# Optimization experiments

Measured on AMD Instinct MI355X. Metric: run time of the kernel, lower is better.

Reference implementation:

```python
import jax, jax.numpy as jnp
import numpy as np

N, V, I, O, G = 16, 4096, 128, 128, 16


def setup_inputs() -> dict:
    key = jax.random.key(0)
    ks = jax.random.split(key, 7)
    stdv = 1.0 / np.sqrt(O)  # reset_parameters: uniform(-stdv, stdv)
    u = lambda k, shape: jax.random.uniform(k, shape, jnp.float32, -stdv, stdv)
    return {
        "x": jax.random.normal(ks[0], (N, V, I), jnp.float32),
        "hx": jax.random.normal(ks[1], (N, V, O), jnp.float32),
        "group_index": jax.random.randint(ks[2], (V,), 0, G),
        "weight_ih": u(ks[3], (3, G, O, I)),
        "bias_ih": u(ks[4], (3, G, O)),
        "weight_hh": u(ks[5], (3, G, O, O)),
        "bias_hh": u(ks[6], (3, G, O)),
    }


def reference(x, hx, group_index, weight_ih, bias_ih, weight_hh, bias_hh):
    # gather per-node weights: [3, V, O, I] / [3, V, O]
    w_ih = weight_ih[:, group_index]
    b_ih = bias_ih[:, group_index]
    w_hh = weight_hh[:, group_index]
    b_hh = bias_hh[:, group_index]

    def lin_x(xx, w, b):  # [N,V,I] x [V,O,I] -> [N,V,O]
        return jnp.einsum("nvi,voi->nvo", xx, w) + b[None]

    def lin_h(h, w, b):  # torch einsum 'NVO,VOO->NVO' takes diagonal of w
        wd = jnp.diagonal(w, axis1=-2, axis2=-1)  # [V,O]
        return h * wd[None] + b[None]

    r = jax.nn.sigmoid(lin_x(x, w_ih[0], b_ih[0]) + lin_h(hx, w_hh[0], b_hh[0]))
    z = jax.nn.sigmoid(lin_x(x, w_ih[1], b_ih[1]) + lin_h(hx, w_hh[1], b_hh[1]))
    n = jnp.tanh(lin_x(x, w_ih[2], b_ih[2]) + r * lin_h(hx, w_hh[2], b_hh[2]))
    return (1.0 - z) * n + z * hx
```

## Files before the change

kernel.cpp:

```cpp
#include <hip/hip_runtime.h>
#include <math.h>

#define NN 16
#define VV 4096
#define II 128
#define OO 128
#define GG 16

typedef __attribute__((ext_vector_type(8))) short bf16x8;
typedef __attribute__((ext_vector_type(4))) float f32x4;

__device__ inline unsigned short f2bf(float f) {
    union { float f; unsigned u; } c; c.f = f;
    unsigned r = c.u + 0x7FFFu + ((c.u >> 16) & 1u);
    return (unsigned short)(r >> 16);
}
__device__ inline float bf2f(unsigned short h) {
    union { unsigned u; float f; } c; c.u = ((unsigned)h) << 16;
    return c.f;
}
__device__ inline void split1(float f, unsigned short& hi, unsigned short& lo) {
    hi = f2bf(f);
    lo = f2bf(f - bf2f(hi));
}
__device__ inline bf16x8 as_bf(uint4 u) {
    union { uint4 u; bf16x8 b; } c; c.u = u; return c.b;
}
__device__ inline void pack8(const float4& a, const float4& b, uint4& ph, uint4& pl) {
    unsigned short hi[8], lo[8];
    split1(a.x, hi[0], lo[0]); split1(a.y, hi[1], lo[1]);
    split1(a.z, hi[2], lo[2]); split1(a.w, hi[3], lo[3]);
    split1(b.x, hi[4], lo[4]); split1(b.y, hi[5], lo[5]);
    split1(b.z, hi[6], lo[6]); split1(b.w, hi[7], lo[7]);
    ph.x = (unsigned)hi[0] | ((unsigned)hi[1] << 16);
    ph.y = (unsigned)hi[2] | ((unsigned)hi[3] << 16);
    ph.z = (unsigned)hi[4] | ((unsigned)hi[5] << 16);
    ph.w = (unsigned)hi[6] | ((unsigned)hi[7] << 16);
    pl.x = (unsigned)lo[0] | ((unsigned)lo[1] << 16);
    pl.y = (unsigned)lo[2] | ((unsigned)lo[3] << 16);
    pl.z = (unsigned)lo[4] | ((unsigned)lo[5] << 16);
    pl.w = (unsigned)lo[6] | ((unsigned)lo[7] << 16);
}

__global__ __launch_bounds__(256) void prepack_kernel(
    const float* __restrict__ w_ih, uint4* __restrict__ wp)
{
    const int t  = blockIdx.x * 256 + threadIdx.x;
    const int i8 = t & 15;
    const int o  = (t >> 4) & 127;
    const int gg = t >> 11;

    const float* src = w_ih + ((size_t)gg * OO + o) * II + i8 * 8;
    const float4 a = *(const float4*)src;
    const float4 b = *(const float4*)(src + 4);
    uint4 ph, pl;
    pack8(a, b, ph, pl);

    const int s    = i8 >> 2;
    const int kb   = i8 & 3;
    const int lane = kb * 16 + (o & 15);
    const int ct   = o >> 4;
    const int pidx = ((gg * 8 + ct) * 4 + s) * 64 + lane;
    wp[pidx * 2]     = ph;
    wp[pidx * 2 + 1] = pl;
}

template <bool PREPACKED>
__global__ __launch_bounds__(256, 4) void ggru_mfma_kernel(
    const float* __restrict__ x,
    const float* __restrict__ hx,
    const int*   __restrict__ gidx,
    const uint4* __restrict__ wp,
    const float* __restrict__ w_ih,
    const float* __restrict__ b_ih,
    const float* __restrict__ w_hh,
    const float* __restrict__ b_hh,
    float*       __restrict__ out)
{
    const int v    = blockIdx.x;
    const int tid  = threadIdx.x;
    const int lane = tid & 63;
    const int wv   = tid >> 6;
    const int g    = gidx[v];

    __shared__ uint4 xhS[256];
    __shared__ uint4 xlS[256];

    {
        const int row = tid >> 4;
        const int sk  = tid & 15;
        const int s   = sk >> 2, kb = sk & 3;
        const float* xp = x + ((size_t)row * VV + v) * II + s * 32 + kb * 8;
        const float4 xa = *(const float4*)xp;
        const float4 xb = *(const float4*)(xp + 4);
        uint4 ph, pl;
        pack8(xa, xb, ph, pl);
        xhS[s * 64 + kb * 16 + row] = ph;
        xlS[s * 64 + kb * 16 + row] = pl;
    }
    __syncthreads();

    int tb[3][2];
    const float* wraw[3][2];
    #pragma unroll
    for (int ga = 0; ga < 3; ++ga) {
        #pragma unroll
        for (int t = 0; t < 2; ++t) {
            const int ct = wv * 2 + t;
            tb[ga][t] = ((ga * GG + g) * 8 + ct) * 4;
            wraw[ga][t] = w_ih + (((size_t)ga * GG + g) * OO + ct * 16 + (lane & 15)) * II
                          + (lane >> 4) * 8;
        }
    }

    f32x4 acc[3][2];
    #pragma unroll
    for (int ga = 0; ga < 3; ++ga)
        #pragma unroll
        for (int t = 0; t < 2; ++t)
            acc[ga][t] = (f32x4){0.f, 0.f, 0.f, 0.f};

    #pragma unroll
    for (int s = 0; s < 4; ++s) {
        const bf16x8 ah = as_bf(xhS[s * 64 + lane]);
        const bf16x8 al = as_bf(xlS[s * 64 + lane]);

        uint4 wh6[6], wl6[6];
        if (PREPACKED) {
            #pragma unroll
            for (int ga = 0; ga < 3; ++ga) {
                #pragma unroll
                for (int t = 0; t < 2; ++t) {
                    const size_t base = (size_t)(tb[ga][t] + s) * 128 + lane * 2;
                    wh6[ga * 2 + t] = wp[base];
                    wl6[ga * 2 + t] = wp[base + 1];
                }
            }
        } else {
            #pragma unroll
            for (int ga = 0; ga < 3; ++ga) {
                #pragma unroll
                for (int t = 0; t < 2; ++t) {
                    const float4 wa = *(const float4*)(wraw[ga][t] + s * 32);
                    const float4 wb = *(const float4*)(wraw[ga][t] + s * 32 + 4);
                    pack8(wa, wb, wh6[ga * 2 + t], wl6[ga * 2 + t]);
                }
            }
        }

        #pragma unroll
        for (int ga = 0; ga < 3; ++ga) {
            #pragma unroll
            for (int t = 0; t < 2; ++t) {
                const bf16x8 wh = as_bf(wh6[ga * 2 + t]);
                const bf16x8 wl = as_bf(wl6[ga * 2 + t]);
                acc[ga][t] = __builtin_amdgcn_mfma_f32_16x16x32_bf16(ah, wh, acc[ga][t], 0, 0, 0);
                acc[ga][t] = __builtin_amdgcn_mfma_f32_16x16x32_bf16(al, wh, acc[ga][t], 0, 0, 0);
                acc[ga][t] = __builtin_amdgcn_mfma_f32_16x16x32_bf16(ah, wl, acc[ga][t], 0, 0, 0);
            }
        }
    }

    const int l15 = lane & 15;
    const int rg  = lane >> 4;
    #pragma unroll
    for (int t = 0; t < 2; ++t) {
        const int o = wv * 32 + t * 16 + l15;

        const float bi0 = b_ih[(0 * GG + g) * OO + o];
        const float bi1 = b_ih[(1 * GG + g) * OO + o];
        const float bi2 = b_ih[(2 * GG + g) * OO + o];
        const float bh0 = b_hh[(0 * GG + g) * OO + o];
        const float bh1 = b_hh[(1 * GG + g) * OO + o];
        const float bh2 = b_hh[(2 * GG + g) * OO + o];
        const float wd0 = w_hh[((size_t)(0 * GG + g) * OO + o) * OO + o];
        const float wd1 = w_hh[((size_t)(1 * GG + g) * OO + o) * OO + o];
        const float wd2 = w_hh[((size_t)(2 * GG + g) * OO + o) * OO + o];

        #pragma unroll
        for (int r = 0; r < 4; ++r) {
            const int row = rg * 4 + r;
            const size_t idx = ((size_t)row * VV + v) * OO + o;
            const float h = hx[idx];

            const float gr  = acc[0][t][r] + bi0 + fmaf(h, wd0, bh0);
            const float gz  = acc[1][t][r] + bi1 + fmaf(h, wd1, bh1);
            const float ghn = fmaf(h, wd2, bh2);

            const float rr = 1.f / (1.f + __expf(-gr));
            const float zz = 1.f / (1.f + __expf(-gz));

            float tt = acc[2][t][r] + bi2 + rr * ghn;
            tt = fminf(fmaxf(tt, -15.f), 15.f);
            const float e2 = __expf(2.f * tt);
            const float th = (e2 - 1.f) / (e2 + 1.f);

            out[idx] = (1.f - zz) * th + zz * h;
        }
    }
}

extern "C" void kernel_launch(void* const* d_in, const int* in_sizes, int n_in,
                              void* d_out, int out_size, void* d_ws, size_t ws_size,
                              hipStream_t stream) {
    const float* x    = (const float*)d_in[0];
    const float* hx   = (const float*)d_in[1];
    const int*   gidx = (const int*)d_in[2];
    const float* w_ih = (const float*)d_in[3];
    const float* b_ih = (const float*)d_in[4];
    const float* w_hh = (const float*)d_in[5];
    const float* b_hh = (const float*)d_in[6];
    float* out = (float*)d_out;
    uint4* wp  = (uint4*)d_ws;

    const size_t need = 98304ull * 32ull;
    if (ws_size >= need) {
        prepack_kernel<<<384, 256, 0, stream>>>(w_ih, wp);
        ggru_mfma_kernel<true><<<VV, 256, 0, stream>>>(
            x, hx, gidx, wp, w_ih, b_ih, w_hh, b_hh, out);
    } else {
        ggru_mfma_kernel<false><<<VV, 256, 0, stream>>>(
            x, hx, gidx, (const uint4*)nullptr, w_ih, b_ih, w_hh, b_hh, out);
    }
}
```

Measured before the change: 172.7 us.

## Bucket nodes by group and share LDS-staged weights across four nodes per block

Adds a single-block bucketing kernel that sorts node indices by group into a padded list, so each 512-thread block processes four nodes from the same group. Per-group prepacked weights are staged once per k-step into LDS and reused by all four nodes, replacing per-node global weight loads and cutting weight traffic about fourfold. In exchange it adds a serial one-block bucket kernel launch, extra __syncthreads per k-step, padding blocks with idle waves, and more LDS use that may limit occupancy.

Result: faster. 162.4 us (-6.0%).

```diff
diff --git a/kernel.cpp b/kernel.cpp
--- a/kernel.cpp
+++ b/kernel.cpp
@@ -6,6 +6,10 @@
 #define II 128
 #define OO 128
 #define GG 16
+
+#define VPB   4
+#define LISTN 4144
+#define NBLK  1036
 
 typedef __attribute__((ext_vector_type(8))) short bf16x8;
 typedef __attribute__((ext_vector_type(4))) float f32x4;
@@ -42,6 +46,29 @@
     pl.w = (unsigned)lo[6] | ((unsigned)lo[7] << 16);
 }
 
+__global__ __launch_bounds__(256) void bucket_kernel(
+    const int* __restrict__ gidx, int* __restrict__ list)
+{
+    __shared__ int cnt[GG], base[GG], cur[GG];
+    const int tid = threadIdx.x;
+    if (tid < GG) cnt[tid] = 0;
+    __syncthreads();
+    for (int v = tid; v < VV; v += 256) atomicAdd(&cnt[gidx[v]], 1);
+    __syncthreads();
+    if (tid == 0) {
+        int o = 0;
+        for (int g = 0; g < GG; ++g) { base[g] = o; o += (cnt[g] + VPB - 1) & ~(VPB - 1); }
+    }
+    __syncthreads();
+    if (tid < GG) cur[tid] = base[tid];
+    for (int i = tid; i < LISTN; i += 256) list[i] = -1;
+    __syncthreads();
+    for (int v = tid; v < VV; v += 256) {
+        const int pos = atomicAdd(&cur[gidx[v]], 1);
+        list[pos] = v;
+    }
+}
+
 __global__ __launch_bounds__(256) void prepack_kernel(
     const float* __restrict__ w_ih, uint4* __restrict__ wp)
 {
@@ -65,17 +92,148 @@
     wp[pidx * 2 + 1] = pl;
 }
 
-template <bool PREPACKED>
-__global__ __launch_bounds__(256, 4) void ggru_mfma_kernel(
+__global__ __launch_bounds__(512, 4) void ggru_gemm_kernel(
     const float* __restrict__ x,
     const float* __restrict__ hx,
     const int*   __restrict__ gidx,
     const uint4* __restrict__ wp,
-    const float* __restrict__ w_ih,
+    const int*   __restrict__ list,
     const float* __restrict__ b_ih,
     const float* __restrict__ w_hh,
     const float* __restrict__ b_hh,
     float*       __restrict__ out)
+{
+    const int b    = blockIdx.x;
+    const int tid  = threadIdx.x;
+    const int lane = tid & 63;
+    const int wv   = tid >> 6;
+    const int vv   = wv >> 1;
+    const int half = wv & 1;
+
+    const int v0 = list[b * VPB];
+    if (v0 < 0) return;
+    const int g = gidx[v0];
+
+    int vl[VPB];
+    #pragma unroll
+    for (int k = 0; k < VPB; ++k) vl[k] = list[b * VPB + k];
+    const int myv = vl[vv];
+
+    __shared__ uint4 xhS[VPB][256];
+    __shared__ uint4 xlS[VPB][256];
+    __shared__ uint4 whS[1536];
+    __shared__ uint4 wlS[1536];
+
+    {
+        const int tv    = tid >> 7;
+        const int inner = tid & 127;
+        const int row   = inner >> 3;
+        const int q     = inner & 7;
+        const int s     = q >> 1;
+        const int kb0   = (q & 1) * 2;
+        const int xv    = vl[tv];
+        if (xv >= 0) {
+            const float* xp = x + ((size_t)row * VV + xv) * II + q * 16;
+            const float4 a0 = ((const float4*)xp)[0];
+            const float4 a1 = ((const float4*)xp)[1];
+            const float4 a2 = ((const float4*)xp)[2];
+            const float4 a3 = ((const float4*)xp)[3];
+            uint4 h0, l0, h1, l1;
+            pack8(a0, a1, h0, l0);
+            pack8(a2, a3, h1, l1);
+            xhS[tv][s * 64 + kb0 * 16 + row]       = h0;
+            xlS[tv][s * 64 + kb0 * 16 + row]       = l0;
+            xhS[tv][s * 64 + (kb0 + 1) * 16 + row] = h1;
+            xlS[tv][s * 64 + (kb0 + 1) * 16 + row] = l1;
+        }
+    }
+
+    f32x4 acc[3][4];
+    #pragma unroll
+    for (int ga = 0; ga < 3; ++ga)
+        #pragma unroll
+        for (int cc = 0; cc < 4; ++cc)
+            acc[ga][cc] = (f32x4){0.f, 0.f, 0.f, 0.f};
+
+    for (int s = 0; s < 4; ++s) {
+        __syncthreads();
+        #pragma unroll
+        for (int j = 0; j < 3; ++j) {
+            const int idx = j * 512 + tid;
+            const int c   = idx >> 6;
+            const int l   = idx & 63;
+            const int ga  = c >> 3;
+            const int ct  = c & 7;
+            const size_t P = ((size_t)(((ga * GG + g) * 8 + ct) * 4 + s)) * 64 + l;
+            whS[idx] = wp[2 * P];
+            wlS[idx] = wp[2 * P + 1];
+        }
+        __syncthreads();
+        if (myv >= 0) {
+            const bf16x8 ah = as_bf(xhS[vv][s * 64 + lane]);
+            const bf16x8 al = as_bf(xlS[vv][s * 64 + lane]);
+            #pragma unroll
+            for (int ga = 0; ga < 3; ++ga) {
+                #pragma unroll
+                for (int cc = 0; cc < 4; ++cc) {
+                    const int c = ga * 8 + half * 4 + cc;
+                    const bf16x8 wh = as_bf(whS[c * 64 + lane]);
+                    const bf16x8 wl = as_bf(wlS[c * 64 + lane]);
+                    acc[ga][cc] = __builtin_amdgcn_mfma_f32_16x16x32_bf16(ah, wh, acc[ga][cc], 0, 0, 0);
+                    acc[ga][cc] = __builtin_amdgcn_mfma_f32_16x16x32_bf16(al, wh, acc[ga][cc], 0, 0, 0);
+                    acc[ga][cc] = __builtin_amdgcn_mfma_f32_16x16x32_bf16(ah, wl, acc[ga][cc], 0, 0, 0);
+                }
+            }
+        }
+    }
+
+    if (myv < 0) return;
+
+    const int l15 = lane & 15;
+    const int rg  = lane >> 4;
+    #pragma unroll
+    for (int cc = 0; cc < 4; ++cc) {
+        const int ct = half * 4 + cc;
+        const int o  = ct * 16 + l15;
+
+        const float bi0 = b_ih[(0 * GG + g) * OO + o];
+        const float bi1 = b_ih[(1 * GG + g) * OO + o];
+        const float bi2 = b_ih[(2 * GG + g) * OO + o];
+        const float bh0 = b_hh[(0 * GG + g) * OO + o];
+        const float bh1 = b_hh[(1 * GG + g) * OO + o];
+        const float bh2 = b_hh[(2 * GG + g) * OO + o];
+        const float wd0 = w_hh[((size_t)(0 * GG + g) * OO + o) * OO + o];
+        const float wd1 = w_hh[((size_t)(1 * GG + g) * OO + o) * OO + o];
+        const float wd2 = w_hh[((size_t)(2 * GG + g) * OO + o) * OO + o];
+
+        #pragma unroll
+        for (int r = 0; r < 4; ++r) {
+            const int row = rg * 4 + r;
+            const size_t idx = ((size_t)row * VV + myv) * OO + o;
+            const float h = hx[idx];
+
+            const float gr  = acc[0][cc][r] + bi0 + fmaf(h, wd0, bh0);
+            const float gz  = acc[1][cc][r] + bi1 + fmaf(h, wd1, bh1);
+            const float ghn = fmaf(h, wd2, bh2);
+
+            const float rr = 1.f / (1.f + __expf(-gr));
+            const float zz = 1.f / (1.f + __expf(-gz));
+
+            float tt = acc[2][cc][r] + bi2 + rr * ghn;
+            tt = fminf(fmaxf(tt, -15.f), 15.f);
+            const float e2 = __expf(2.f * tt);
+            const float th = (e2 - 1.f) / (e2 + 1.f);
+
+            out[idx] = (1.f - zz) * th + zz * h;
+        }
+    }
+}
+
+__global__ __launch_bounds__(256, 4) void ggru_fallback_kernel(
+    const float* __restrict__ x, const float* __restrict__ hx,
+    const int* __restrict__ gidx, const float* __restrict__ w_ih,
+    const float* __restrict__ b_ih, const float* __restrict__ w_hh,
+    const float* __restrict__ b_hh, float* __restrict__ out)
 {
     const int v    = blockIdx.x;
     const int tid  = threadIdx.x;
@@ -100,18 +258,15 @@
     }
     __syncthreads();
 
-    int tb[3][2];
     const float* wraw[3][2];
     #pragma unroll
-    for (int ga = 0; ga < 3; ++ga) {
+    for (int ga = 0; ga < 3; ++ga)
         #pragma unroll
         for (int t = 0; t < 2; ++t) {
             const int ct = wv * 2 + t;
-            tb[ga][t] = ((ga * GG + g) * 8 + ct) * 4;
             wraw[ga][t] = w_ih + (((size_t)ga * GG + g) * OO + ct * 16 + (lane & 15)) * II
                           + (lane >> 4) * 8;
         }
-    }
 
     f32x4 acc[3][2];
     #pragma unroll
@@ -124,41 +279,20 @@
     for (int s = 0; s < 4; ++s) {
         const bf16x8 ah = as_bf(xhS[s * 64 + lane]);
         const bf16x8 al = as_bf(xlS[s * 64 + lane]);
-
-        uint4 wh6[6], wl6[6];
-        if (PREPACKED) {
-            #pragma unroll
-            for (int ga = 0; ga < 3; ++ga) {
-                #pragma unroll
-                for (int t = 0; t < 2; ++t) {
-                    const size_t base = (size_t)(tb[ga][t] + s) * 128 + lane * 2;
-                    wh6[ga * 2 + t] = wp[base];
-                    wl6[ga * 2 + t] = wp[base + 1];
-                }
-            }
-        } else {
-            #pragma unroll
-            for (int ga = 0; ga < 3; ++ga) {
-                #pragma unroll
-                for (int t = 0; t < 2; ++t) {
-                    const float4 wa = *(const float4*)(wraw[ga][t] + s * 32);
-                    const float4 wb = *(const float4*)(wraw[ga][t] + s * 32 + 4);
-                    pack8(wa, wb, wh6[ga * 2 + t], wl6[ga * 2 + t]);
-                }
-            }
-        }
-
-        #pragma unroll
-        for (int ga = 0; ga < 3; ++ga) {
+        #pragma unroll
+        for (int ga = 0; ga < 3; ++ga)
             #pragma unroll
             for (int t = 0; t < 2; ++t) {
-                const bf16x8 wh = as_bf(wh6[ga * 2 + t]);
-                const bf16x8 wl = as_bf(wl6[ga * 2 + t]);
+                const float4 wa = *(const float4*)(wraw[ga][t] + s * 32);
+                const float4 wb = *(const float4*)(wraw[ga][t] + s * 32 + 4);
+                uint4 ph, pl;
+                pack8(wa, wb, ph, pl);
+                const bf16x8 wh = as_bf(ph);
+                const bf16x8 wl = as_bf(pl);
                 acc[ga][t] = __builtin_amdgcn_mfma_f32_16x16x32_bf16(ah, wh, acc[ga][t], 0, 0, 0);
                 acc[ga][t] = __builtin_amdgcn_mfma_f32_16x16x32_bf16(al, wh, acc[ga][t], 0, 0, 0);
                 acc[ga][t] = __builtin_amdgcn_mfma_f32_16x16x32_bf16(ah, wl, acc[ga][t], 0, 0, 0);
             }
-        }
     }
 
     const int l15 = lane & 15;
@@ -166,7 +300,6 @@
     #pragma unroll
     for (int t = 0; t < 2; ++t) {
         const int o = wv * 32 + t * 16 + l15;
-
         const float bi0 = b_ih[(0 * GG + g) * OO + o];
         const float bi1 = b_ih[(1 * GG + g) * OO + o];
         const float bi2 = b_ih[(2 * GG + g) * OO + o];
@@ -176,25 +309,20 @@
         const float wd0 = w_hh[((size_t)(0 * GG + g) * OO + o) * OO + o];
         const float wd1 = w_hh[((size_t)(1 * GG + g) * OO + o) * OO + o];
         const float wd2 = w_hh[((size_t)(2 * GG + g) * OO + o) * OO + o];
-
         #pragma unroll
         for (int r = 0; r < 4; ++r) {
             const int row = rg * 4 + r;
             const size_t idx = ((size_t)row * VV + v) * OO + o;
             const float h = hx[idx];
-
             const float gr  = acc[0][t][r] + bi0 + fmaf(h, wd0, bh0);
             const float gz  = acc[1][t][r] + bi1 + fmaf(h, wd1, bh1);
             const float ghn = fmaf(h, wd2, bh2);
-
             const float rr = 1.f / (1.f + __expf(-gr));
             const float zz = 1.f / (1.f + __expf(-gz));
-
             float tt = acc[2][t][r] + bi2 + rr * ghn;
             tt = fminf(fmaxf(tt, -15.f), 15.f);
             const float e2 = __expf(2.f * tt);
             const float th = (e2 - 1.f) / (e2 + 1.f);
-
             out[idx] = (1.f - zz) * th + zz * h;
         }
     }
@@ -211,15 +339,19 @@
     const float* w_hh = (const float*)d_in[5];
     const float* b_hh = (const float*)d_in[6];
     float* out = (float*)d_out;
+
+    const size_t wp_bytes  = 98304ull * 32ull;
+    const size_t need      = wp_bytes + LISTN * sizeof(int);
     uint4* wp  = (uint4*)d_ws;
-
-    const size_t need = 98304ull * 32ull;
+    int*  list = (int*)((char*)d_ws + wp_bytes);
+
     if (ws_size >= need) {
+        bucket_kernel<<<1, 256, 0, stream>>>(gidx, list);
         prepack_kernel<<<384, 256, 0, stream>>>(w_ih, wp);
-        ggru_mfma_kernel<true><<<VV, 256, 0, stream>>>(
-            x, hx, gidx, wp, w_ih, b_ih, w_hh, b_hh, out);
+        ggru_gemm_kernel<<<NBLK, 512, 0, stream>>>(
+            x, hx, gidx, wp, list, b_ih, w_hh, b_hh, out);
     } else {
-        ggru_mfma_kernel<false><<<VV, 256, 0, stream>>>(
-            x, hx, gidx, (const uint4*)nullptr, w_ih, b_ih, w_hh, b_hh, out);
-    }
-}
+        ggru_fallback_kernel<<<VV, 256, 0, stream>>>(
+            x, hx, gidx, w_ih, b_ih, w_hh, b_hh, out);
+    }
+}
```
